# Optimization experiments

Hardware: AMD Instinct MI355X
Metric: run time of the kernel (lower is better)

## Reference

```python
import jax, jax.numpy as jnp
import numpy as np

LN_EPS = 1e-5

def setup_inputs() -> dict:
    key = jax.random.key(0)
    ks = jax.random.split(key, 4)
    B, D, H, K = 8192, 4096, 2048, 512
    return {
        "x": jax.random.normal(ks[0], (B, D), jnp.float32),
        "beta": jax.random.normal(ks[1], (D, K), jnp.float32) * 0.01,
        "compound_mean": jnp.zeros((D,), jnp.float32),
        "W1": jax.random.normal(ks[2], (H, D), jnp.float32) * 0.02,
        "b1": jnp.zeros((H,), jnp.float32),
        "ln_w": jnp.ones((H,), jnp.float32),
        "ln_b": jnp.zeros((H,), jnp.float32),
        "W2": jax.random.normal(ks[3], (K, H), jnp.float32) * 0.02,
        "b2": jnp.zeros((K,), jnp.float32),
    }

def reference(x, beta, compound_mean, W1, b1, ln_w, ln_b, W2, b2):
    # compound path of BiQBMVAE.forward (compound=True)
    h = jnp.einsum('bd,hd->bh', x - compound_mean, W1) + b1      # fc1
    mu = jnp.mean(h, axis=-1, keepdims=True)                      # LayerNorm
    var = jnp.mean(jnp.square(h - mu), axis=-1, keepdims=True)
    h = (h - mu) * jax.lax.rsqrt(var + LN_EPS) * ln_w + ln_b
    h = jax.nn.relu(h)                                            # act_fn
    q_logits = jnp.einsum('bh,kh->bk', h, W2) + b2                # fc2 -> [B, k]
    x_recon = jax.nn.sigmoid(jnp.einsum('bk,dk->bd', q_logits, beta))  # decode_compound
    return (q_logits, x_recon, q_logits, q_logits)
```

## Files before the change

### kernel.cpp

```cpp
#include <hip/hip_runtime.h>
#include <hip/hip_bf16.h>
#include <cstddef>
#include <cstdint>

#define LN_EPS 1e-5f

#define B_DIM 8192
#define D_DIM 4096
#define H_DIM 2048
#define K_DIM 512

typedef __bf16 bf16x8_t __attribute__((ext_vector_type(8)));
typedef float f32x4_t __attribute__((ext_vector_type(4)));

__device__ __forceinline__ void gl2lds16(const __hip_bfloat16* g,
                                         __hip_bfloat16* l) {
  __builtin_amdgcn_global_load_lds(
      (const __attribute__((address_space(1))) uint32_t*)g,
      (__attribute__((address_space(3))) uint32_t*)l, 16, 0, 0);
}

__global__ __launch_bounds__(256) void conv_x_kernel(
    const float* __restrict__ x, const float* __restrict__ cmean,
    __hip_bfloat16* __restrict__ out) {
  const long i = (((long)blockIdx.x << 8) + threadIdx.x) << 3;
  const int col = (int)(i & (D_DIM - 1));
  const float4 a = *(const float4*)(x + i);
  const float4 b = *(const float4*)(x + i + 4);
  const float4 ma = *(const float4*)(cmean + col);
  const float4 mb = *(const float4*)(cmean + col + 4);
  union { __hip_bfloat16 h[8]; uint4 u; } pk;
  pk.h[0] = __float2bfloat16(a.x - ma.x);
  pk.h[1] = __float2bfloat16(a.y - ma.y);
  pk.h[2] = __float2bfloat16(a.z - ma.z);
  pk.h[3] = __float2bfloat16(a.w - ma.w);
  pk.h[4] = __float2bfloat16(b.x - mb.x);
  pk.h[5] = __float2bfloat16(b.y - mb.y);
  pk.h[6] = __float2bfloat16(b.z - mb.z);
  pk.h[7] = __float2bfloat16(b.w - mb.w);
  *(uint4*)(out + i) = pk.u;
}

__global__ __launch_bounds__(256) void conv_w3_kernel(
    const float* __restrict__ W1, const float* __restrict__ W2,
    const float* __restrict__ beta, __hip_bfloat16* __restrict__ W1b,
    __hip_bfloat16* __restrict__ W2b, __hip_bfloat16* __restrict__ betab) {
  const int blk = blockIdx.x;
  const float* src;
  __hip_bfloat16* dst;
  long base;
  if (blk < 4096) {
    src = W1; dst = W1b; base = blk;
  } else if (blk < 4608) {
    src = W2; dst = W2b; base = blk - 4096;
  } else {
    src = beta; dst = betab; base = blk - 4608;
  }
  const long i = ((base << 8) + threadIdx.x) << 3;
  const float4 a = *(const float4*)(src + i);
  const float4 b = *(const float4*)(src + i + 4);
  union { __hip_bfloat16 h[8]; uint4 u; } pk;
  pk.h[0] = __float2bfloat16(a.x);
  pk.h[1] = __float2bfloat16(a.y);
  pk.h[2] = __float2bfloat16(a.z);
  pk.h[3] = __float2bfloat16(a.w);
  pk.h[4] = __float2bfloat16(b.x);
  pk.h[5] = __float2bfloat16(b.y);
  pk.h[6] = __float2bfloat16(b.z);
  pk.h[7] = __float2bfloat16(b.w);
  *(uint4*)(dst + i) = pk.u;
}

template <int EPI>
__global__ __launch_bounds__(512, 2) void gemm256_ring(
    const __hip_bfloat16* __restrict__ A, int lda,
    const __hip_bfloat16* __restrict__ Bm, int ldb,
    const float* __restrict__ bias, float* __restrict__ C0, int ldc, int Kd) {
  constexpr int SLOT = 16384;
  __shared__ __hip_bfloat16 lds[4 * SLOT];

  const int t_ = threadIdx.x;
  const int lane = t_ & 63;
  const int wv = t_ >> 6;
  const int wr = wv >> 2;
  const int wc = wv & 3;
  const int fr = lane & 15;
  const int ko = lane >> 4;
  const int kos = (ko ^ ((fr >> 1) & 3)) * 8;

  const int gx = gridDim.x;
  const int nwg = gx * gridDim.y;
  const int f = blockIdx.y * gx + blockIdx.x;
  const int w = (f & 7) * (nwg >> 3) + (f >> 3);
  const int bx = w % gx;
  const int by = w / gx;

  const long rowA = (long)by * 256;
  const long rowB = (long)bx * 256;

  const int ci = (wv << 6) + lane;
  const int srow = ci >> 2;
  const int skq = (ci & 3) ^ ((ci >> 3) & 3);
  const __hip_bfloat16* sA0 = A + (rowA + srow) * (long)lda + skq * 8;
  const __hip_bfloat16* sA1 = sA0 + 128L * lda;
  const __hip_bfloat16* sB0 = Bm + (rowB + srow) * (long)ldb + skq * 8;
  const __hip_bfloat16* sB1 = sB0 + 128L * ldb;

  auto STG = [&](int s, int k0) {
    __hip_bfloat16* d = lds + s * SLOT + wv * 512;
    gl2lds16(sA0 + k0, d);
    gl2lds16(sA1 + k0, d + 4096);
    gl2lds16(sB0 + k0, d + 8192);
    gl2lds16(sB1 + k0, d + 12288);
  };

  f32x4_t acc[8][4];
  const f32x4_t zero = {0.f, 0.f, 0.f, 0.f};
#pragma unroll
  for (int a = 0; a < 8; ++a)
#pragma unroll
    for (int b = 0; b < 4; ++b) acc[a][b] = zero;

  const int NT = Kd >> 5;

  STG(0, 0);
  STG(1, 32);
  STG(2, 64);
  asm volatile("s_waitcnt vmcnt(4)" ::: "memory");
  __builtin_amdgcn_s_barrier();
  __builtin_amdgcn_sched_barrier(0);

  bf16x8_t F0a[4], F0b[4], F1a[4], F1b[4];
#pragma unroll
  for (int mi = 0; mi < 4; ++mi)
    F0a[mi] = *(const bf16x8_t*)&lds[(wr * 128 + mi * 16 + fr) * 32 + kos];
#pragma unroll
  for (int ni = 0; ni < 4; ++ni)
    F0b[ni] =
        *(const bf16x8_t*)&lds[8192 + (wc * 64 + ni * 16 + fr) * 32 + kos];

  auto BODY = [&](int t, bf16x8_t(&cf)[4], bf16x8_t(&cb)[4],
                  bf16x8_t(&nf)[4], bf16x8_t(&nb)[4]) {
    const int st = (t & 3) * SLOT;
    if (t + 3 < NT) STG((t + 3) & 3, (t + 3) * 32);
    bf16x8_t ag[4];
#pragma unroll
    for (int mi = 0; mi < 4; ++mi)
      ag[mi] =
          *(const bf16x8_t*)&lds[st + (wr * 128 + 64 + mi * 16 + fr) * 32 +
                                 kos];
    if (t + 1 < NT) {
      const int s1 = ((t + 1) & 3) * SLOT;
#pragma unroll
      for (int mi = 0; mi < 4; ++mi)
        nf[mi] =
            *(const bf16x8_t*)&lds[s1 + (wr * 128 + mi * 16 + fr) * 32 + kos];
#pragma unroll
      for (int ni = 0; ni < 4; ++ni)
        nb[ni] = *(const bf16x8_t*)&lds[s1 + 8192 +
                                        (wc * 64 + ni * 16 + fr) * 32 + kos];
    }
    __builtin_amdgcn_s_setprio(1);
#pragma unroll
    for (int mi = 0; mi < 4; ++mi)
#pragma unroll
      for (int ni = 0; ni < 4; ++ni)
        acc[mi][ni] = __builtin_amdgcn_mfma_f32_16x16x32_bf16(
            cf[mi], cb[ni], acc[mi][ni], 0, 0, 0);
#pragma unroll
    for (int mi = 0; mi < 4; ++mi)
#pragma unroll
      for (int ni = 0; ni < 4; ++ni)
        acc[4 + mi][ni] = __builtin_amdgcn_mfma_f32_16x16x32_bf16(
            ag[mi], cb[ni], acc[4 + mi][ni], 0, 0, 0);
    __builtin_amdgcn_s_setprio(0);
    if (t + 1 < NT) {
      if (t + 3 < NT)
        asm volatile("s_waitcnt vmcnt(4)" ::: "memory");
      else
        asm volatile("s_waitcnt vmcnt(0)" ::: "memory");
      __builtin_amdgcn_s_barrier();
      __builtin_amdgcn_sched_barrier(0);
    }
  };

  for (int t = 0; t < NT; t += 2) {
    BODY(t, F0a, F0b, F1a, F1b);
    BODY(t + 1, F1a, F1b, F0a, F0b);
  }

  const long cRow0 = rowA + wr * 128;
  const int cCol0 = (int)rowB + wc * 64;
#pragma unroll
  for (int a = 0; a < 8; ++a) {
#pragma unroll
    for (int b = 0; b < 4; ++b) {
      f32x4_t v4 = acc[a][b];
      const int col = cCol0 + b * 16 + fr;
#pragma unroll
      for (int r = 0; r < 4; ++r) {
        const long row = cRow0 + a * 16 + ko * 4 + r;
        float val = v4[r];
        if constexpr (EPI == 0) {
          val += bias[col];
        } else {
          val = 1.f / (1.f + __expf(-val));
        }
        C0[row * (long)ldc + col] = val;
      }
    }
  }
}

template <int EPI>
__global__ __launch_bounds__(512, 4) void gemm128_ring(
    const __hip_bfloat16* __restrict__ A, int lda,
    const __hip_bfloat16* __restrict__ Bm, int ldb,
    const float* __restrict__ bias, float* __restrict__ C0, int ldc,
    float* __restrict__ C2, float* __restrict__ C3,
    __hip_bfloat16* __restrict__ Cb, int Kd) {
  constexpr int SLOT = 8192;
  __shared__ __hip_bfloat16 lds[4 * SLOT];

  const int t_ = threadIdx.x;
  const int lane = t_ & 63;
  const int wv = t_ >> 6;
  const int wr = wv >> 2;
  const int wc = wv & 3;
  const int fr = lane & 15;
  const int ko = lane >> 4;
  const int kos = (ko ^ ((fr >> 1) & 3)) * 8;

  const int gx = gridDim.x;
  const int nwg = gx * gridDim.y;
  const int f = blockIdx.y * gx + blockIdx.x;
  const int w = (f & 7) * (nwg >> 3) + (f >> 3);
  const int bx = w % gx;
  const int by = w / gx;

  const long rowA = (long)by * 128;
  const long rowB = (long)bx * 128;

  const int ci = (wv << 6) + lane;
  const int srow = ci >> 2;
  const int skq = (ci & 3) ^ ((ci >> 3) & 3);
  const __hip_bfloat16* sA = A + (rowA + srow) * (long)lda + skq * 8;
  const __hip_bfloat16* sB = Bm + (rowB + srow) * (long)ldb + skq * 8;

  auto STG = [&](int s, int k0) {
    __hip_bfloat16* d = lds + s * SLOT + wv * 512;
    gl2lds16(sA + k0, d);
    gl2lds16(sB + k0, d + 4096);
  };

  f32x4_t acc[4][2];
  const f32x4_t zero = {0.f, 0.f, 0.f, 0.f};
#pragma unroll
  for (int a = 0; a < 4; ++a)
#pragma unroll
    for (int b = 0; b < 2; ++b) acc[a][b] = zero;

  const int NT = Kd >> 5;

  STG(0, 0);
  STG(1, 32);
  STG(2, 64);
  asm volatile("s_waitcnt vmcnt(2)" ::: "memory");
  __builtin_amdgcn_s_barrier();
  __builtin_amdgcn_sched_barrier(0);

  bf16x8_t F0a[4], F0b[2], F1a[4], F1b[2];
#pragma unroll
  for (int mi = 0; mi < 4; ++mi)
    F0a[mi] = *(const bf16x8_t*)&lds[(wr * 64 + mi * 16 + fr) * 32 + kos];
#pragma unroll
  for (int ni = 0; ni < 2; ++ni)
    F0b[ni] =
        *(const bf16x8_t*)&lds[4096 + (wc * 32 + ni * 16 + fr) * 32 + kos];

  auto BODY = [&](int t, bf16x8_t(&cf)[4], bf16x8_t(&cb)[2],
                  bf16x8_t(&nf)[4], bf16x8_t(&nb)[2]) {
    if (t + 3 < NT) STG((t + 3) & 3, (t + 3) * 32);
    if (t + 1 < NT) {
      const int s1 = ((t + 1) & 3) * SLOT;
#pragma unroll
      for (int mi = 0; mi < 4; ++mi)
        nf[mi] =
            *(const bf16x8_t*)&lds[s1 + (wr * 64 + mi * 16 + fr) * 32 + kos];
#pragma unroll
      for (int ni = 0; ni < 2; ++ni)
        nb[ni] = *(const bf16x8_t*)&lds[s1 + 4096 +
                                        (wc * 32 + ni * 16 + fr) * 32 + kos];
    }
    __builtin_amdgcn_s_setprio(1);
#pragma unroll
    for (int mi = 0; mi < 4; ++mi)
#pragma unroll
      for (int ni = 0; ni < 2; ++ni)
        acc[mi][ni] = __builtin_amdgcn_mfma_f32_16x16x32_bf16(
            cf[mi], cb[ni], acc[mi][ni], 0, 0, 0);
    __builtin_amdgcn_s_setprio(0);
    if (t + 1 < NT) {
      if (t + 3 < NT)
        asm volatile("s_waitcnt vmcnt(2)" ::: "memory");
      else
        asm volatile("s_waitcnt vmcnt(0)" ::: "memory");
      __builtin_amdgcn_s_barrier();
      __builtin_amdgcn_sched_barrier(0);
    }
  };

  for (int t = 0; t < NT; t += 2) {
    BODY(t, F0a, F0b, F1a, F1b);
    BODY(t + 1, F1a, F1b, F0a, F0b);
  }

  const long cRow0 = rowA + wr * 64;
  const int cCol0 = (int)rowB + wc * 32;
#pragma unroll
  for (int a = 0; a < 4; ++a) {
#pragma unroll
    for (int b = 0; b < 2; ++b) {
      f32x4_t v4 = acc[a][b];
      const int col = cCol0 + b * 16 + fr;
#pragma unroll
      for (int r = 0; r < 4; ++r) {
        const long row = cRow0 + a * 16 + ko * 4 + r;
        float val = v4[r];
        if constexpr (EPI == 1) {
          val += bias[col];
          C0[row * (long)ldc + col] = val;
          C2[row * (long)ldc + col] = val;
          C3[row * (long)ldc + col] = val;
          Cb[row * (long)ldc + col] = __float2bfloat16(val);
        } else {
          val = 1.f / (1.f + __expf(-val));
          C0[row * (long)ldc + col] = val;
        }
      }
    }
  }
}

__global__ __launch_bounds__(256) void ln_relu_kernel(
    void* hptr, const float* __restrict__ ln_w, const float* __restrict__ ln_b) {
  const int H = H_DIM;
  float* h = (float*)hptr;
  __hip_bfloat16* hb = (__hip_bfloat16*)hptr;

  const long row = blockIdx.x;
  const int t = threadIdx.x;
  const int lane = t & 63;
  const int wv = t >> 6;
  const float* hr = h + row * H;

  float v[8];
#pragma unroll
  for (int i = 0; i < 8; ++i) v[i] = hr[t + i * 256];

  __shared__ float red[8];

  float s = 0.f;
#pragma unroll
  for (int i = 0; i < 8; ++i) s += v[i];
#pragma unroll
  for (int off = 32; off; off >>= 1) s += __shfl_down(s, off);
  if (lane == 0) red[wv] = s;
  __syncthreads();
  const float mu = (red[0] + red[1] + red[2] + red[3]) * (1.f / (float)H);

  float vs = 0.f;
#pragma unroll
  for (int i = 0; i < 8; ++i) {
    float d = v[i] - mu;
    vs += d * d;
  }
#pragma unroll
  for (int off = 32; off; off >>= 1) vs += __shfl_down(vs, off);
  if (lane == 0) red[4 + wv] = vs;
  __syncthreads();
  const float var = (red[4] + red[5] + red[6] + red[7]) * (1.f / (float)H);
  const float rs = rsqrtf(var + LN_EPS);

  __hip_bfloat16* hbr = hb + row * (long)D_DIM;
#pragma unroll
  for (int i = 0; i < 8; ++i) {
    int col = t + i * 256;
    float y = (v[i] - mu) * rs * ln_w[col] + ln_b[col];
    y = fmaxf(y, 0.f);
    hbr[col] = __float2bfloat16(y);
  }
}

extern "C" void kernel_launch(void* const* d_in, const int* in_sizes, int n_in,
                              void* d_out, int out_size, void* d_ws,
                              size_t ws_size, hipStream_t stream) {
  const float* x = (const float*)d_in[0];
  const float* beta = (const float*)d_in[1];
  const float* cmean = (const float*)d_in[2];
  const float* W1 = (const float*)d_in[3];
  const float* b1 = (const float*)d_in[4];
  const float* ln_w = (const float*)d_in[5];
  const float* ln_b = (const float*)d_in[6];
  const float* W2 = (const float*)d_in[7];
  const float* b2 = (const float*)d_in[8];

  float* out = (float*)d_out;
  float* q0 = out;
  float* xr = out + (size_t)B_DIM * K_DIM;
  float* q2 = xr + (size_t)B_DIM * D_DIM;
  float* q3 = q2 + (size_t)B_DIM * K_DIM;

  __hip_bfloat16* xb = (__hip_bfloat16*)xr;
  float* h = xr + (size_t)B_DIM * D_DIM / 2;
  __hip_bfloat16* hb = (__hip_bfloat16*)h;

  __hip_bfloat16* W1b = (__hip_bfloat16*)d_ws;
  __hip_bfloat16* W2b = W1b + (size_t)H_DIM * D_DIM;
  __hip_bfloat16* betab = W2b + (size_t)K_DIM * H_DIM;
  __hip_bfloat16* qb = betab + (size_t)D_DIM * K_DIM;

  dim3 blk(256, 1, 1);
  dim3 blk512(512, 1, 1);

  hipLaunchKernelGGL(conv_x_kernel, dim3((B_DIM * (size_t)D_DIM) / 2048), blk,
                     0, stream, x, cmean, xb);
  hipLaunchKernelGGL(conv_w3_kernel, dim3(4096 + 512 + 1024), blk, 0, stream,
                     W1, W2, beta, W1b, W2b, betab);

  hipLaunchKernelGGL((gemm256_ring<0>), dim3(H_DIM / 256, B_DIM / 256),
                     blk512, 0, stream, xb, D_DIM, W1b, D_DIM, b1, h, H_DIM,
                     D_DIM);

  hipLaunchKernelGGL(ln_relu_kernel, dim3(B_DIM), blk, 0, stream, (void*)h,
                     ln_w, ln_b);

  hipLaunchKernelGGL((gemm128_ring<1>), dim3(K_DIM / 128, B_DIM / 128),
                     blk512, 0, stream, hb, D_DIM, W2b, H_DIM, b2, q0, K_DIM,
                     q2, q3, qb, H_DIM);

  hipLaunchKernelGGL((gemm128_ring<2>), dim3(D_DIM / 128, B_DIM / 128),
                     blk512, 0, stream, qb, K_DIM, betab, K_DIM,
                     (const float*)nullptr, xr, D_DIM, (float*)nullptr,
                     (float*)nullptr, (__hip_bfloat16*)nullptr, K_DIM);
}
```

Before: 534.1 us.

## Load GEMM B operand directly to registers, merge conversion kernels, vectorize LayerNorm

The fc1 GEMM stops staging the weight tile through LDS: each wave loads its B fragments straight from global memory into registers with a one-step prefetch, halving LDS use and LDS read traffic. The two fp32-to-bf16 conversion kernels are merged into a single launch, and the LayerNorm kernel uses contiguous vector loads and stores. The direct global B loads are strided and duplicated across waves, and they have less latency hiding than the LDS ring, so stalls may increase.

```diff
diff --git a/kernel.cpp b/kernel.cpp
--- a/kernel.cpp
+++ b/kernel.cpp
@@ -20,41 +20,42 @@
       (__attribute__((address_space(3))) uint32_t*)l, 16, 0, 0);
 }
 
-__global__ __launch_bounds__(256) void conv_x_kernel(
+__global__ __launch_bounds__(256) void conv_all_kernel(
     const float* __restrict__ x, const float* __restrict__ cmean,
-    __hip_bfloat16* __restrict__ out) {
-  const long i = (((long)blockIdx.x << 8) + threadIdx.x) << 3;
-  const int col = (int)(i & (D_DIM - 1));
-  const float4 a = *(const float4*)(x + i);
-  const float4 b = *(const float4*)(x + i + 4);
-  const float4 ma = *(const float4*)(cmean + col);
-  const float4 mb = *(const float4*)(cmean + col + 4);
-  union { __hip_bfloat16 h[8]; uint4 u; } pk;
-  pk.h[0] = __float2bfloat16(a.x - ma.x);
-  pk.h[1] = __float2bfloat16(a.y - ma.y);
-  pk.h[2] = __float2bfloat16(a.z - ma.z);
-  pk.h[3] = __float2bfloat16(a.w - ma.w);
-  pk.h[4] = __float2bfloat16(b.x - mb.x);
-  pk.h[5] = __float2bfloat16(b.y - mb.y);
-  pk.h[6] = __float2bfloat16(b.z - mb.z);
-  pk.h[7] = __float2bfloat16(b.w - mb.w);
-  *(uint4*)(out + i) = pk.u;
-}
-
-__global__ __launch_bounds__(256) void conv_w3_kernel(
-    const float* __restrict__ W1, const float* __restrict__ W2,
-    const float* __restrict__ beta, __hip_bfloat16* __restrict__ W1b,
-    __hip_bfloat16* __restrict__ W2b, __hip_bfloat16* __restrict__ betab) {
+    __hip_bfloat16* __restrict__ xb, const float* __restrict__ W1,
+    const float* __restrict__ W2, const float* __restrict__ beta,
+    __hip_bfloat16* __restrict__ W1b, __hip_bfloat16* __restrict__ W2b,
+    __hip_bfloat16* __restrict__ betab) {
   const int blk = blockIdx.x;
+  if (blk < 16384) {
+    const long i = (((long)blk << 8) + threadIdx.x) << 3;
+    const int col = (int)(i & (D_DIM - 1));
+    const float4 a = *(const float4*)(x + i);
+    const float4 b = *(const float4*)(x + i + 4);
+    const float4 ma = *(const float4*)(cmean + col);
+    const float4 mb = *(const float4*)(cmean + col + 4);
+    union { __hip_bfloat16 h[8]; uint4 u; } pk;
+    pk.h[0] = __float2bfloat16(a.x - ma.x);
+    pk.h[1] = __float2bfloat16(a.y - ma.y);
+    pk.h[2] = __float2bfloat16(a.z - ma.z);
+    pk.h[3] = __float2bfloat16(a.w - ma.w);
+    pk.h[4] = __float2bfloat16(b.x - mb.x);
+    pk.h[5] = __float2bfloat16(b.y - mb.y);
+    pk.h[6] = __float2bfloat16(b.z - mb.z);
+    pk.h[7] = __float2bfloat16(b.w - mb.w);
+    *(uint4*)(xb + i) = pk.u;
+    return;
+  }
+  const int b2 = blk - 16384;
   const float* src;
   __hip_bfloat16* dst;
   long base;
-  if (blk < 4096) {
-    src = W1; dst = W1b; base = blk;
-  } else if (blk < 4608) {
-    src = W2; dst = W2b; base = blk - 4096;
+  if (b2 < 4096) {
+    src = W1; dst = W1b; base = b2;
+  } else if (b2 < 4608) {
+    src = W2; dst = W2b; base = b2 - 4096;
   } else {
-    src = beta; dst = betab; base = blk - 4608;
+    src = beta; dst = betab; base = b2 - 4608;
   }
   const long i = ((base << 8) + threadIdx.x) << 3;
   const float4 a = *(const float4*)(src + i);
@@ -72,11 +73,11 @@
 }
 
 template <int EPI>
-__global__ __launch_bounds__(512, 2) void gemm256_ring(
+__global__ __launch_bounds__(512, 2) void gemm256_bg(
     const __hip_bfloat16* __restrict__ A, int lda,
     const __hip_bfloat16* __restrict__ Bm, int ldb,
     const float* __restrict__ bias, float* __restrict__ C0, int ldc, int Kd) {
-  constexpr int SLOT = 16384;
+  constexpr int SLOT = 8192;
   __shared__ __hip_bfloat16 lds[4 * SLOT];
 
   const int t_ = threadIdx.x;
@@ -103,16 +104,15 @@
   const int skq = (ci & 3) ^ ((ci >> 3) & 3);
   const __hip_bfloat16* sA0 = A + (rowA + srow) * (long)lda + skq * 8;
   const __hip_bfloat16* sA1 = sA0 + 128L * lda;
-  const __hip_bfloat16* sB0 = Bm + (rowB + srow) * (long)ldb + skq * 8;
-  const __hip_bfloat16* sB1 = sB0 + 128L * ldb;
 
   auto STG = [&](int s, int k0) {
     __hip_bfloat16* d = lds + s * SLOT + wv * 512;
     gl2lds16(sA0 + k0, d);
     gl2lds16(sA1 + k0, d + 4096);
-    gl2lds16(sB0 + k0, d + 8192);
-    gl2lds16(sB1 + k0, d + 12288);
   };
+
+  const __hip_bfloat16* pB = Bm + (rowB + wc * 64 + fr) * (long)ldb + ko * 8;
+  const long bStep = 16L * ldb;
 
   f32x4_t acc[8][4];
   const f32x4_t zero = {0.f, 0.f, 0.f, 0.f};
@@ -123,42 +123,46 @@
 
   const int NT = Kd >> 5;
 
+  bf16x8_t cb[4], nb[4];
+#pragma unroll
+  for (int ni = 0; ni < 4; ++ni)
+    cb[ni] = *(const bf16x8_t*)(pB + ni * bStep);
   STG(0, 0);
   STG(1, 32);
   STG(2, 64);
-  asm volatile("s_waitcnt vmcnt(4)" ::: "memory");
+  asm volatile("s_waitcnt vmcnt(2)" ::: "memory");
   __builtin_amdgcn_s_barrier();
   __builtin_amdgcn_sched_barrier(0);
 
-  bf16x8_t F0a[4], F0b[4], F1a[4], F1b[4];
+  bf16x8_t F0a[4], F1a[4];
 #pragma unroll
   for (int mi = 0; mi < 4; ++mi)
     F0a[mi] = *(const bf16x8_t*)&lds[(wr * 128 + mi * 16 + fr) * 32 + kos];
-#pragma unroll
-  for (int ni = 0; ni < 4; ++ni)
-    F0b[ni] =
-        *(const bf16x8_t*)&lds[8192 + (wc * 64 + ni * 16 + fr) * 32 + kos];
-
-  auto BODY = [&](int t, bf16x8_t(&cf)[4], bf16x8_t(&cb)[4],
-                  bf16x8_t(&nf)[4], bf16x8_t(&nb)[4]) {
+
+  auto BODY = [&](int t, bf16x8_t(&cf)[4], bf16x8_t(&cbv)[4],
+                  bf16x8_t(&nf)[4], bf16x8_t(&nbv)[4]) {
     const int st = (t & 3) * SLOT;
-    if (t + 3 < NT) STG((t + 3) & 3, (t + 3) * 32);
+    const bool pfA = (t + 3) < NT;
+    const bool pfB = (t + 1) < NT;
+    if (pfA) STG((t + 3) & 3, (t + 3) * 32);
+    if (pfB) {
+      const int kk = (t + 1) * 32;
+#pragma unroll
+      for (int ni = 0; ni < 4; ++ni)
+        nbv[ni] = *(const bf16x8_t*)(pB + ni * bStep + kk);
+    }
     bf16x8_t ag[4];
 #pragma unroll
     for (int mi = 0; mi < 4; ++mi)
       ag[mi] =
           *(const bf16x8_t*)&lds[st + (wr * 128 + 64 + mi * 16 + fr) * 32 +
                                  kos];
-    if (t + 1 < NT) {
+    if (pfB) {
       const int s1 = ((t + 1) & 3) * SLOT;
 #pragma unroll
       for (int mi = 0; mi < 4; ++mi)
         nf[mi] =
             *(const bf16x8_t*)&lds[s1 + (wr * 128 + mi * 16 + fr) * 32 + kos];
-#pragma unroll
-      for (int ni = 0; ni < 4; ++ni)
-        nb[ni] = *(const bf16x8_t*)&lds[s1 + 8192 +
-                                        (wc * 64 + ni * 16 + fr) * 32 + kos];
     }
     __builtin_amdgcn_s_setprio(1);
 #pragma unroll
@@ -166,27 +170,27 @@
 #pragma unroll
       for (int ni = 0; ni < 4; ++ni)
         acc[mi][ni] = __builtin_amdgcn_mfma_f32_16x16x32_bf16(
-            cf[mi], cb[ni], acc[mi][ni], 0, 0, 0);
+            cf[mi], cbv[ni], acc[mi][ni], 0, 0, 0);
 #pragma unroll
     for (int mi = 0; mi < 4; ++mi)
 #pragma unroll
       for (int ni = 0; ni < 4; ++ni)
         acc[4 + mi][ni] = __builtin_amdgcn_mfma_f32_16x16x32_bf16(
-            ag[mi], cb[ni], acc[4 + mi][ni], 0, 0, 0);
+            ag[mi], cbv[ni], acc[4 + mi][ni], 0, 0, 0);
     __builtin_amdgcn_s_setprio(0);
-    if (t + 1 < NT) {
-      if (t + 3 < NT)
+    if (pfB) {
+      if (pfA)
+        asm volatile("s_waitcnt vmcnt(6)" ::: "memory");
+      else
         asm volatile("s_waitcnt vmcnt(4)" ::: "memory");
-      else
-        asm volatile("s_waitcnt vmcnt(0)" ::: "memory");
       __builtin_amdgcn_s_barrier();
       __builtin_amdgcn_sched_barrier(0);
     }
   };
 
   for (int t = 0; t < NT; t += 2) {
-    BODY(t, F0a, F0b, F1a, F1b);
-    BODY(t + 1, F1a, F1b, F0a, F0b);
+    BODY(t, F0a, cb, F1a, nb);
+    BODY(t + 1, F1a, nb, F0a, cb);
   }
 
   const long cRow0 = rowA + wr * 128;
@@ -352,11 +356,11 @@
   const int t = threadIdx.x;
   const int lane = t & 63;
   const int wv = t >> 6;
-  const float* hr = h + row * H;
-
-  float v[8];
-#pragma unroll
-  for (int i = 0; i < 8; ++i) v[i] = hr[t + i * 256];
+  const float* hr = h + row * H + t * 8;
+
+  const float4 va = *(const float4*)hr;
+  const float4 vb = *(const float4*)(hr + 4);
+  float v[8] = {va.x, va.y, va.z, va.w, vb.x, vb.y, vb.z, vb.w};
 
   __shared__ float red[8];
 
@@ -382,14 +386,20 @@
   const float var = (red[4] + red[5] + red[6] + red[7]) * (1.f / (float)H);
   const float rs = rsqrtf(var + LN_EPS);
 
-  __hip_bfloat16* hbr = hb + row * (long)D_DIM;
+  const float4 wa = *(const float4*)(ln_w + t * 8);
+  const float4 wb = *(const float4*)(ln_w + t * 8 + 4);
+  const float4 ba = *(const float4*)(ln_b + t * 8);
+  const float4 bb = *(const float4*)(ln_b + t * 8 + 4);
+  const float wgt[8] = {wa.x, wa.y, wa.z, wa.w, wb.x, wb.y, wb.z, wb.w};
+  const float bia[8] = {ba.x, ba.y, ba.z, ba.w, bb.x, bb.y, bb.z, bb.w};
+
+  union { __hip_bfloat16 hh[8]; uint4 u; } pk;
 #pragma unroll
   for (int i = 0; i < 8; ++i) {
-    int col = t + i * 256;
-    float y = (v[i] - mu) * rs * ln_w[col] + ln_b[col];
-    y = fmaxf(y, 0.f);
-    hbr[col] = __float2bfloat16(y);
-  }
+    float y = (v[i] - mu) * rs * wgt[i] + bia[i];
+    pk.hh[i] = __float2bfloat16(fmaxf(y, 0.f));
+  }
+  *(uint4*)(hb + row * (long)D_DIM + t * 8) = pk.u;
 }
 
 extern "C" void kernel_launch(void* const* d_in, const int* in_sizes, int n_in,
@@ -423,14 +433,11 @@
   dim3 blk(256, 1, 1);
   dim3 blk512(512, 1, 1);
 
-  hipLaunchKernelGGL(conv_x_kernel, dim3((B_DIM * (size_t)D_DIM) / 2048), blk,
-                     0, stream, x, cmean, xb);
-  hipLaunchKernelGGL(conv_w3_kernel, dim3(4096 + 512 + 1024), blk, 0, stream,
-                     W1, W2, beta, W1b, W2b, betab);
-
-  hipLaunchKernelGGL((gemm256_ring<0>), dim3(H_DIM / 256, B_DIM / 256),
-                     blk512, 0, stream, xb, D_DIM, W1b, D_DIM, b1, h, H_DIM,
-                     D_DIM);
+  hipLaunchKernelGGL(conv_all_kernel, dim3(16384 + 4096 + 512 + 1024), blk, 0,
+                     stream, x, cmean, xb, W1, W2, beta, W1b, W2b, betab);
+
+  hipLaunchKernelGGL((gemm256_bg<0>), dim3(H_DIM / 256, B_DIM / 256), blk512,
+                     0, stream, xb, D_DIM, W1b, D_DIM, b1, h, H_DIM, D_DIM);
 
   hipLaunchKernelGGL(ln_relu_kernel, dim3(B_DIM), blk, 0, stream, (void*)h,
                      ln_w, ln_b);
```

Measured after the change: 590.2 us. 10.5% more time.
